# Performance work log

Hardware: AMD Instinct MI355X
Metric: run time of the kernel (lower is better)

The kernel has to match this reference:

```python
import jax, jax.numpy as jnp
import numpy as np

A = 4096      # alleles
RPA = 20      # mean reads per allele
R = A * RPA   # total reads per data source
C = 12        # input channels (pileup features)
L = 32        # read window length
D = 32        # hidden feature dim
NOUT = 2


def setup_inputs() -> dict:
    key = jax.random.key(0)
    k = jax.random.split(key, 8)
    # ragged read counts per allele (alternating 16/24, mean 20, sums to R)
    counts0 = np.tile(np.array([16, 24], dtype=np.int64), A // 2)
    counts1 = np.tile(np.array([24, 16], dtype=np.int64), A // 2)
    return {
        "tensors0": jax.random.normal(k[0], (R, C, L), dtype=jnp.float32),
        "tensors1": jax.random.normal(k[1], (R, C, L), dtype=jnp.float32),
        "W0": jax.random.normal(k[2], (D, C), dtype=jnp.float32) * 0.1,
        "b0": jnp.zeros((D,), dtype=jnp.float32),
        "W1": jax.random.normal(k[3], (D, C), dtype=jnp.float32) * 0.1,
        "b1": jnp.zeros((D,), dtype=jnp.float32),
        "W2": jax.random.normal(k[4], (NOUT, 2 * D), dtype=jnp.float32) * 0.1,
        "b2": jnp.zeros((NOUT,), dtype=jnp.float32),
        "numReadsPerAllele0": jnp.asarray(counts0),
        "numReadsPerAllele1": jnp.asarray(counts1),
        "numAllelesPerSite": jnp.full((A // 2,), 2, dtype=jnp.int64),
        "depthMultiplier0": jnp.asarray(counts0, dtype=jnp.float32),
        "depthMultiplier1": jnp.asarray(counts1, dtype=jnp.float32),
    }


def _frames(t, W, b):
    # pointwise read-feature extractor: [R,C,L] -> [R,D,L]
    return jax.nn.relu(jnp.einsum('rcl,dc->rdl', t, W) + b[None, :, None])


def reference(tensors0, tensors1, W0, b0, W1, b1, W2, b2,
              numReadsPerAllele0, numReadsPerAllele1,
              numAllelesPerSite, depthMultiplier0, depthMultiplier1):
    nA = numReadsPerAllele0.shape[0]
    nR = tensors0.shape[0]
    # segment ids replace torch.split + per-segment torch.sum (ragged segment-sum)
    seg0 = jnp.repeat(jnp.arange(nA), numReadsPerAllele0, total_repeat_length=nR)
    seg1 = jnp.repeat(jnp.arange(nA), numReadsPerAllele1, total_repeat_length=nR)

    frames0 = _frames(tensors0, W0, b0)  # [R,D,L]
    frames1 = _frames(tensors1, W1, b1)

    red0 = jax.ops.segment_sum(frames0, seg0, num_segments=nA)  # [A,D,L]
    red1 = jax.ops.segment_sum(frames1, seg1, num_segments=nA)

    # depth normalization (normalize() in the original)
    red0 = red0 / depthMultiplier0[:, None, None]
    red1 = red1 / depthMultiplier1[:, None, None]

    reduced = jnp.concatenate((red0, red1), axis=1)  # [A, 2D, L]

    # network2 (GraphSearcher): site-specific head modeled as pool + linear
    pooled = jnp.mean(reduced, axis=2)               # [A, 2D]
    return pooled @ W2.T + b2                        # [A, NOUT]
```

## Files before the change

kernel.cpp:

```cpp
#include <hip/hip_runtime.h>

#define A_ALLELES 4096
#define CCH 12
#define LW 32
#define DH 32
#define RDF (CCH * LW)

typedef __attribute__((ext_vector_type(8)))  short bf16x8;
typedef __attribute__((ext_vector_type(16))) float f32x16;

__device__ inline unsigned pk2(float fa, float fb) {
    const unsigned a = __float_as_uint(fa), b = __float_as_uint(fb);
    return ((a + 0x8000u) >> 16) | ((b + 0x8000u) & 0xffff0000u);
}

__global__ __launch_bounds__(256) void scan_kernel(
    const int* __restrict__ c0, const int* __restrict__ c1,
    int* __restrict__ o0, int* __restrict__ o1)
{
    const int* c = (blockIdx.x == 0) ? c0 : c1;
    int*       o = (blockIdx.x == 0) ? o0 : o1;

    __shared__ int part[256];
    const int tid  = threadIdx.x;
    const int base = tid * 16;

    int loc[16];
    int s = 0;
#pragma unroll
    for (int i = 0; i < 16; ++i) { loc[i] = c[base + i]; s += loc[i]; }
    part[tid] = s;
    __syncthreads();

    for (int st = 1; st < 256; st <<= 1) {
        int v = (tid >= st) ? part[tid - st] : 0;
        __syncthreads();
        part[tid] += v;
        __syncthreads();
    }

    int excl = (tid == 0) ? 0 : part[tid - 1];
#pragma unroll
    for (int i = 0; i < 16; ++i) { o[base + i] = excl; excl += loc[i]; }
}

__global__ __launch_bounds__(256, 4) void main_kernel(
    const float* __restrict__ t0, const float* __restrict__ t1,
    const float* __restrict__ W0, const float* __restrict__ b0,
    const float* __restrict__ W1, const float* __restrict__ b1,
    const float* __restrict__ W2, const float* __restrict__ b2,
    const int*  __restrict__ cnt0, const int* __restrict__ cnt1,
    const float* __restrict__ dm0, const float* __restrict__ dm1,
    const int*  __restrict__ offs0, const int* __restrict__ offs1,
    float* __restrict__ out)
{
    __shared__ float sW2[2 * 2 * DH];
    __shared__ float sB2[2];

    const int tid = threadIdx.x;
    if (tid < 2 * 2 * DH) sW2[tid] = W2[tid];
    if (tid < 2) sB2[tid] = b2[tid];
    __syncthreads();

    const int w    = tid >> 6;
    const int lane = tid & 63;
    const int src  = blockIdx.x >> 10;
    const int a    = ((blockIdx.x & 1023) << 2) | w;

    const float* __restrict__ tens = src ? t1 : t0;
    const int*   __restrict__ cnt  = src ? cnt1 : cnt0;
    const int*   __restrict__ offs = src ? offs1 : offs0;
    const float* __restrict__ dm   = src ? dm1 : dm0;
    const float* __restrict__ gW   = src ? W1 : W0;
    const float* __restrict__ gB   = src ? b1 : b0;

    const int l = lane & 31;
    const int h = lane >> 5;

    union { bf16x8 v; unsigned u[4]; } Af;
#pragma unroll
    for (int p = 0; p < 4; ++p) {
        const int c0 = h * 8 + 2 * p, c1 = c0 + 1;
        const float f0 = (c0 < CCH) ? gW[l * CCH + c0] : 0.f;
        const float f1 = (c1 < CCH) ? gW[l * CCH + c1] : 0.f;
        Af.u[p] = pk2(f0, f1);
    }
    f32x16 cb;
#pragma unroll
    for (int reg = 0; reg < 16; ++reg)
        cb[reg] = gB[(reg & 3) + 8 * (reg >> 2) + 4 * h];

    const int n     = cnt[a];
    const int start = offs[a];
    const float* rb = tens + (size_t)start * RDF;

    const float* pLo = rb + l + h * 256;
    const float* pHi = rb + l + (h ? 256 : 128);

    float acc[16];
#pragma unroll
    for (int reg = 0; reg < 16; ++reg) acc[reg] = 0.f;

#define LOAD8(buf, P, W_)  do {                                     \
        buf[0] = pLo[(P) + 0];  buf[1] = pLo[(P) + 32];             \
        buf[2] = pLo[(P) + 64]; buf[3] = pLo[(P) + 96];             \
        buf[4] = pHi[(P) + 0];  buf[5] = pHi[(P) + 32];             \
        buf[6] = pHi[(P) + 64]; buf[7] = pHi[(P) + 96]; } while (0)

#define PACK_MFMA_ACC(buf) do {                                     \
        union { bf16x8 v; unsigned u[4]; } Bf;                      \
        Bf.u[0] = pk2(buf[0], buf[1]); Bf.u[1] = pk2(buf[2], buf[3]); \
        Bf.u[2] = pk2(buf[4], buf[5]); Bf.u[3] = pk2(buf[6], buf[7]); \
        const f32x16 D = __builtin_amdgcn_mfma_f32_32x32x16_bf16(   \
            Af.v, Bf.v, cb, 0, 0, 0);                               \
        _Pragma("unroll")                                           \
        for (int reg = 0; reg < 16; ++reg)                          \
            acc[reg] += fmaxf(D[reg], 0.f); } while (0)

    const int n2 = n & ~1;
    if (n2 >= 2) {
        float bA[8], bB[8];
        LOAD8(bA, 0, 0);
        LOAD8(bB, 384, 0);
        const int iters = (n2 - 2) >> 1;
        for (int it = 0; it < iters; ++it) {
            {
                union { bf16x8 v; unsigned u[4]; } Bf;
                Bf.u[0] = pk2(bA[0], bA[1]); Bf.u[1] = pk2(bA[2], bA[3]);
                Bf.u[2] = pk2(bA[4], bA[5]); Bf.u[3] = pk2(bA[6], bA[7]);
                LOAD8(bA, 768, 0);
                const f32x16 D = __builtin_amdgcn_mfma_f32_32x32x16_bf16(
                    Af.v, Bf.v, cb, 0, 0, 0);
#pragma unroll
                for (int reg = 0; reg < 16; ++reg) acc[reg] += fmaxf(D[reg], 0.f);
                pLo += 384; pHi += 384;
            }
            {
                union { bf16x8 v; unsigned u[4]; } Bf;
                Bf.u[0] = pk2(bB[0], bB[1]); Bf.u[1] = pk2(bB[2], bB[3]);
                Bf.u[2] = pk2(bB[4], bB[5]); Bf.u[3] = pk2(bB[6], bB[7]);
                LOAD8(bB, 768, 0);
                const f32x16 D = __builtin_amdgcn_mfma_f32_32x32x16_bf16(
                    Af.v, Bf.v, cb, 0, 0, 0);
#pragma unroll
                for (int reg = 0; reg < 16; ++reg) acc[reg] += fmaxf(D[reg], 0.f);
                pLo += 384; pHi += 384;
            }
        }
        PACK_MFMA_ACC(bA);
        PACK_MFMA_ACC(bB);
    }
    if (n & 1) {
        const float* qLo = rb + (size_t)(n - 1) * RDF + l + h * 256;
        const float* qHi = rb + (size_t)(n - 1) * RDF + l + (h ? 256 : 128);
        float bT[8];
        bT[0] = qLo[0];  bT[1] = qLo[32]; bT[2] = qLo[64]; bT[3] = qLo[96];
        bT[4] = qHi[0];  bT[5] = qHi[32]; bT[6] = qHi[64]; bT[7] = qHi[96];
        PACK_MFMA_ACC(bT);
    }

#pragma unroll
    for (int reg = 0; reg < 16; ++reg) {
#pragma unroll
        for (int mm = 1; mm < 32; mm <<= 1)
            acc[reg] += __shfl_xor(acc[reg], mm, 64);
    }

    const float scale = 1.f / (32.f * dm[a]);
    float c0s = 0.f, c1s = 0.f;
#pragma unroll
    for (int reg = 0; reg < 16; ++reg) {
        const int d = (reg & 3) + 8 * (reg >> 2) + 4 * h;
        const float pv = acc[reg] * scale;
        c0s = fmaf(pv, sW2[0 * 2 * DH + src * DH + d], c0s);
        c1s = fmaf(pv, sW2[1 * 2 * DH + src * DH + d], c1s);
    }
    c0s += __shfl_xor(c0s, 32, 64);
    c1s += __shfl_xor(c1s, 32, 64);

    if (lane == 0) {
        if (src == 0) { c0s += sB2[0]; c1s += sB2[1]; }
        atomicAdd(&out[a * 2 + 0], c0s);
        atomicAdd(&out[a * 2 + 1], c1s);
    }
#undef LOAD8
#undef PACK_MFMA_ACC
}

extern "C" void kernel_launch(void* const* d_in, const int* in_sizes, int n_in,
                              void* d_out, int out_size, void* d_ws, size_t ws_size,
                              hipStream_t stream) {
    const float* t0  = (const float*)d_in[0];
    const float* t1  = (const float*)d_in[1];
    const float* W0  = (const float*)d_in[2];
    const float* b0  = (const float*)d_in[3];
    const float* W1  = (const float*)d_in[4];
    const float* b1  = (const float*)d_in[5];
    const float* W2  = (const float*)d_in[6];
    const float* b2  = (const float*)d_in[7];
    const int*  cnt0 = (const int*)d_in[8];
    const int*  cnt1 = (const int*)d_in[9];
    const float* dm0 = (const float*)d_in[11];
    const float* dm1 = (const float*)d_in[12];

    int* offs0 = (int*)d_ws;
    int* offs1 = offs0 + A_ALLELES;

    hipMemsetAsync(d_out, 0, (size_t)out_size * sizeof(float), stream);
    scan_kernel<<<2, 256, 0, stream>>>(cnt0, cnt1, offs0, offs1);

    main_kernel<<<2048, 256, 0, stream>>>(
        t0, t1, W0, b0, W1, b1, W2, b2,
        cnt0, cnt1, dm0, dm1, offs0, offs1, (float*)d_out);
}
```

Baseline: 293.7 us.

## Stage read chunks through LDS with async global_load_lds double buffering

Replaces per-lane strided global loads with 16-byte global_load_lds transfers that bring two reads at a time into a per-wave double-buffered LDS staging area. The MFMA operands are then read from LDS, and packing uses the hardware v_cvt_pk_bf16_f32 instruction. The aim is fully coalesced 16-byte global traffic and loads that overlap with compute. In exchange it adds 24KB of LDS per block, which may limit occupancy, and relies on hand-written vmcnt/lgkmcnt waits for correctness.

```diff
diff --git a/kernel.cpp b/kernel.cpp
--- a/kernel.cpp
+++ b/kernel.cpp
@@ -5,6 +5,7 @@
 #define LW 32
 #define DH 32
 #define RDF (CCH * LW)
+#define CHF (2 * RDF)
 
 typedef __attribute__((ext_vector_type(8)))  short bf16x8;
 typedef __attribute__((ext_vector_type(16))) float f32x16;
@@ -13,6 +14,16 @@
     const unsigned a = __float_as_uint(fa), b = __float_as_uint(fb);
     return ((a + 0x8000u) >> 16) | ((b + 0x8000u) & 0xffff0000u);
 }
+
+__device__ inline unsigned cvtpk(float lo, float hi) {
+    unsigned r;
+    asm("v_cvt_pk_bf16_f32 %0, %1, %2" : "=v"(r) : "v"(lo), "v"(hi));
+    return r;
+}
+
+#define GLD16(gp, lp) __builtin_amdgcn_global_load_lds(                   \
+        (const __attribute__((address_space(1))) void*)(gp),              \
+        (__attribute__((address_space(3))) void*)(lp), 16, 0, 0)
 
 __global__ __launch_bounds__(256) void scan_kernel(
     const int* __restrict__ c0, const int* __restrict__ c1,
@@ -56,6 +67,7 @@
 {
     __shared__ float sW2[2 * 2 * DH];
     __shared__ float sB2[2];
+    __shared__ float stg[4][2][CHF];
 
     const int tid = threadIdx.x;
     if (tid < 2 * 2 * DH) sW2[tid] = W2[tid];
@@ -94,84 +106,88 @@
     const int start = offs[a];
     const float* rb = tens + (size_t)start * RDF;
 
-    const float* pLo = rb + l + h * 256;
-    const float* pHi = rb + l + (h ? 256 : 128);
-
     float acc[16];
 #pragma unroll
-    for (int reg = 0; reg < 16; ++reg) acc[reg] = 0.f;
-
-#define LOAD8(buf, P, W_)  do {                                     \
-        buf[0] = pLo[(P) + 0];  buf[1] = pLo[(P) + 32];             \
-        buf[2] = pLo[(P) + 64]; buf[3] = pLo[(P) + 96];             \
-        buf[4] = pHi[(P) + 0];  buf[5] = pHi[(P) + 32];             \
-        buf[6] = pHi[(P) + 64]; buf[7] = pHi[(P) + 96]; } while (0)
-
-#define PACK_MFMA_ACC(buf) do {                                     \
-        union { bf16x8 v; unsigned u[4]; } Bf;                      \
-        Bf.u[0] = pk2(buf[0], buf[1]); Bf.u[1] = pk2(buf[2], buf[3]); \
-        Bf.u[2] = pk2(buf[4], buf[5]); Bf.u[3] = pk2(buf[6], buf[7]); \
-        const f32x16 D = __builtin_amdgcn_mfma_f32_32x32x16_bf16(   \
-            Af.v, Bf.v, cb, 0, 0, 0);                               \
-        _Pragma("unroll")                                           \
-        for (int reg = 0; reg < 16; ++reg)                          \
-            acc[reg] += fmaxf(D[reg], 0.f); } while (0)
-
-    const int n2 = n & ~1;
-    if (n2 >= 2) {
-        float bA[8], bB[8];
-        LOAD8(bA, 0, 0);
-        LOAD8(bB, 384, 0);
-        const int iters = (n2 - 2) >> 1;
-        for (int it = 0; it < iters; ++it) {
-            {
+    for (int r = 0; r < 16; ++r) acc[r] = 0.f;
+
+    const int base0 = h * 256 + l;
+
+    const int nch = (n & ~1) >> 1;
+
+    if (nch > 0) {
+        {
+            const float* g = rb + (size_t)lane * 4;
+            GLD16(g,       &stg[w][0][0]);
+            GLD16(g + 256, &stg[w][0][256]);
+            GLD16(g + 512, &stg[w][0][512]);
+        }
+        if (nch > 1) {
+            const float* g = rb + CHF + (size_t)lane * 4;
+            GLD16(g,       &stg[w][1][0]);
+            GLD16(g + 256, &stg[w][1][256]);
+            GLD16(g + 512, &stg[w][1][512]);
+        }
+        for (int ch = 0; ch < nch; ++ch) {
+            const int cur = ch & 1;
+            if (ch + 1 < nch) { asm volatile("s_waitcnt vmcnt(3)" ::: "memory"); }
+            else              { asm volatile("s_waitcnt vmcnt(0)" ::: "memory"); }
+#pragma unroll
+            for (int q = 0; q < 2; ++q) {
+                const int off  = q * RDF + base0;
+                const int off2 = off + (h ? 0 : 128);
+                const float v0 = stg[w][cur][off];
+                const float v1 = stg[w][cur][off + 32];
+                const float v2 = stg[w][cur][off + 64];
+                const float v3 = stg[w][cur][off + 96];
+                const float v4 = stg[w][cur][off2];
+                const float v5 = stg[w][cur][off2 + 32];
+                const float v6 = stg[w][cur][off2 + 64];
+                const float v7 = stg[w][cur][off2 + 96];
                 union { bf16x8 v; unsigned u[4]; } Bf;
-                Bf.u[0] = pk2(bA[0], bA[1]); Bf.u[1] = pk2(bA[2], bA[3]);
-                Bf.u[2] = pk2(bA[4], bA[5]); Bf.u[3] = pk2(bA[6], bA[7]);
-                LOAD8(bA, 768, 0);
+                Bf.u[0] = cvtpk(v0, v1); Bf.u[1] = cvtpk(v2, v3);
+                Bf.u[2] = cvtpk(v4, v5); Bf.u[3] = cvtpk(v6, v7);
                 const f32x16 D = __builtin_amdgcn_mfma_f32_32x32x16_bf16(
                     Af.v, Bf.v, cb, 0, 0, 0);
 #pragma unroll
-                for (int reg = 0; reg < 16; ++reg) acc[reg] += fmaxf(D[reg], 0.f);
-                pLo += 384; pHi += 384;
+                for (int r = 0; r < 16; ++r) acc[r] += fmaxf(D[r], 0.f);
             }
-            {
-                union { bf16x8 v; unsigned u[4]; } Bf;
-                Bf.u[0] = pk2(bB[0], bB[1]); Bf.u[1] = pk2(bB[2], bB[3]);
-                Bf.u[2] = pk2(bB[4], bB[5]); Bf.u[3] = pk2(bB[6], bB[7]);
-                LOAD8(bB, 768, 0);
-                const f32x16 D = __builtin_amdgcn_mfma_f32_32x32x16_bf16(
-                    Af.v, Bf.v, cb, 0, 0, 0);
-#pragma unroll
-                for (int reg = 0; reg < 16; ++reg) acc[reg] += fmaxf(D[reg], 0.f);
-                pLo += 384; pHi += 384;
+            if (ch + 2 < nch) {
+                asm volatile("s_waitcnt lgkmcnt(0)" ::: "memory");
+                const float* g = rb + (size_t)(ch + 2) * CHF + (size_t)lane * 4;
+                GLD16(g,       &stg[w][cur][0]);
+                GLD16(g + 256, &stg[w][cur][256]);
+                GLD16(g + 512, &stg[w][cur][512]);
             }
         }
-        PACK_MFMA_ACC(bA);
-        PACK_MFMA_ACC(bB);
-    }
+    }
+
     if (n & 1) {
         const float* qLo = rb + (size_t)(n - 1) * RDF + l + h * 256;
         const float* qHi = rb + (size_t)(n - 1) * RDF + l + (h ? 256 : 128);
-        float bT[8];
-        bT[0] = qLo[0];  bT[1] = qLo[32]; bT[2] = qLo[64]; bT[3] = qLo[96];
-        bT[4] = qHi[0];  bT[5] = qHi[32]; bT[6] = qHi[64]; bT[7] = qHi[96];
-        PACK_MFMA_ACC(bT);
-    }
-
-#pragma unroll
-    for (int reg = 0; reg < 16; ++reg) {
+        const float u0 = qLo[0],  u1 = qLo[32], u2 = qLo[64], u3 = qLo[96];
+        const float u4 = qHi[0],  u5 = qHi[32], u6 = qHi[64], u7 = qHi[96];
+        union { bf16x8 v; unsigned u[4]; } Bf;
+        Bf.u[0] = pk2(u0, u1); Bf.u[1] = pk2(u2, u3);
+        Bf.u[2] = pk2(u4, u5); Bf.u[3] = pk2(u6, u7);
+        const f32x16 D = __builtin_amdgcn_mfma_f32_32x32x16_bf16(
+            Af.v, Bf.v, cb, 0, 0, 0);
+#pragma unroll
+        for (int r = 0; r < 16; ++r) acc[r] += fmaxf(D[r], 0.f);
+    }
+
+#pragma unroll
+    for (int r = 0; r < 16; ++r) {
 #pragma unroll
         for (int mm = 1; mm < 32; mm <<= 1)
-            acc[reg] += __shfl_xor(acc[reg], mm, 64);
+            acc[r] += __shfl_xor(acc[r], mm, 64);
     }
 
     const float scale = 1.f / (32.f * dm[a]);
     float c0s = 0.f, c1s = 0.f;
 #pragma unroll
-    for (int reg = 0; reg < 16; ++reg) {
-        const int d = (reg & 3) + 8 * (reg >> 2) + 4 * h;
-        const float pv = acc[reg] * scale;
+    for (int r = 0; r < 16; ++r) {
+        const int d = (r & 3) + 8 * (r >> 2) + 4 * h;
+        const float pv = acc[r] * scale;
         c0s = fmaf(pv, sW2[0 * 2 * DH + src * DH + d], c0s);
         c1s = fmaf(pv, sW2[1 * 2 * DH + src * DH + d], c1s);
     }
@@ -183,8 +199,6 @@
         atomicAdd(&out[a * 2 + 0], c0s);
         atomicAdd(&out[a * 2 + 1], c1s);
     }
-#undef LOAD8
-#undef PACK_MFMA_ACC
 }
 
 extern "C" void kernel_launch(void* const* d_in, const int* in_sizes, int n_in,
```

Result: no change. 296.2 us (+0.9%).
